# Kernel optimization log

Measured on AMD Instinct MI355X. Metric: run time of the kernel, lower is better.

The kernel has to match this reference:

```python
import jax, jax.numpy as jnp
import numpy as np

D = 1024   # cfg.hid (downscaled from 8192)
M = 20000  # cfg.mem_c // 2 (downscaled)
B, LQ = 4, 8
PLAST_S = 0.05
IMPORTANCE = 1.0


def mha_shared_kv(q, kv_k, kv_v, Wi, bi, Wo, bo, nheads):
    """torch nn.MultiheadAttention (batch_first) with batch-shared K/V.
    q: [B,Lq,D]; kv_k/kv_v: [Lk,D] shared across batch (avoids the .repeat()
    materialization in the original torch code while computing identical math)."""
    dh = D // nheads
    Wq, Wk, Wv = jnp.split(Wi, 3, axis=0)
    bq, bk, bv = jnp.split(bi, 3)
    qp = (jnp.einsum('bqd,ed->bqe', q, Wq) + bq) * (dh ** -0.5)
    kp = kv_k @ Wk.T + bk              # [Lk,D]
    vp = kv_v @ Wv.T + bv              # [Lk,D]
    qh = qp.reshape(q.shape[0], q.shape[1], nheads, dh)      # [B,Lq,h,dh]
    kh = kp.reshape(kp.shape[0], nheads, dh)                 # [Lk,h,dh]
    vh = vp.reshape(vp.shape[0], nheads, dh)                 # [Lk,h,dh]
    scores = jnp.einsum('bqhd,khd->bhqk', qh, kh)            # [B,h,Lq,Lk]
    attn = jax.nn.softmax(scores, axis=-1)
    ctx = jnp.einsum('bhqk,khd->bqhd', attn, vh)
    ctx = ctx.reshape(q.shape[0], q.shape[1], D)
    return ctx @ Wo.T + bo


def setup_inputs() -> dict:
    key = jax.random.key(0)
    ks = jax.random.split(key, 16)
    s = 0.02
    return {
        'q':    jax.random.normal(ks[0], (B, LQ, D), jnp.float32),
        'data': jax.random.normal(ks[1], (B, D), jnp.float32),
        'ek':   jax.random.normal(ks[2], (M, D), jnp.float32),
        'ev':   jax.random.normal(ks[3], (M, D), jnp.float32),
        'sk':   jax.random.normal(ks[4], (M, D), jnp.float32),
        'sv':   jax.random.normal(ks[5], (M, D), jnp.float32),
        'wm':   jax.random.normal(ks[6], (10, D), jnp.float32),
        'Wi_e': jax.random.normal(ks[7], (3 * D, D), jnp.float32) * s,
        'bi_e': jnp.zeros((3 * D,), jnp.float32),
        'Wo_e': jax.random.normal(ks[8], (D, D), jnp.float32) * s,
        'bo_e': jnp.zeros((D,), jnp.float32),
        'Wi_s': jax.random.normal(ks[9], (3 * D, D), jnp.float32) * s,
        'bi_s': jnp.zeros((3 * D,), jnp.float32),
        'Wo_s': jax.random.normal(ks[10], (D, D), jnp.float32) * s,
        'bo_s': jnp.zeros((D,), jnp.float32),
        'Wi_w': jax.random.normal(ks[11], (3 * D, D), jnp.float32) * s,
        'bi_w': jnp.zeros((3 * D,), jnp.float32),
        'Wo_w': jax.random.normal(ks[12], (D, D), jnp.float32) * s,
        'bo_w': jnp.zeros((D,), jnp.float32),
        'Wrp':  jax.random.normal(ks[13], (D, 3 * D), jnp.float32) * s,
        'brp':  jnp.zeros((D,), jnp.float32),
        'eu':   jnp.zeros((M,), jnp.float32),
    }


def reference(q, data, ek, ev, sk, sv, wm,
              Wi_e, bi_e, Wo_e, bo_e,
              Wi_s, bi_s, Wo_s, bo_s,
              Wi_w, bi_w, Wo_w, bo_w,
              Wrp, brp, eu):
    # ---- NeuroMemory.read ----
    e_r = mha_shared_kv(q, ek, ev, Wi_e, bi_e, Wo_e, bo_e, 16)
    s_r = mha_shared_kv(q, sk, sv, Wi_s, bi_s, Wo_s, bo_s, 16)
    w_r = mha_shared_kv(q, wm, wm, Wi_w, bi_w, Wo_w, bo_w, 8)
    read_out = jnp.concatenate([e_r, s_r, w_r], axis=-1) @ Wrp.T + brp  # [B,Lq,D]

    # ---- NeuroMemory.write (episodic, Hebbian plasticity update) ----
    scores = data @ ek.T                       # [B,M]
    probs = jax.nn.softmax(scores, axis=-1)    # [B,M]
    upd = probs * (PLAST_S * IMPORTANCE)       # [B,M]
    u = upd.mean(axis=0)[:, None]              # [M,1] (batch-mean update strength)
    d = data.mean(axis=0)[None, :]             # [1,D]
    new_ek = ek * (1.0 - u) + d * u            # [M,D]
    new_ev = ev * (1.0 - u) + d * u            # [M,D]
    new_eu = eu * 0.99 + jax.lax.stop_gradient(probs.sum(axis=0))  # [M]
    return (read_out, new_ek, new_ev, new_eu)
```

## Files before the change

kernel.cpp:

```cpp
#include <hip/hip_runtime.h>
#include <hip/hip_fp16.h>
#include <hip/hip_bf16.h>
#include <cstdint>
#include <cstddef>

#define D_HID 1024
#define MEM_M 20000
#define NBATCH 4
#define BL 32
#define NROWS 512
#define SROWS_E 516
#define SROWS_S 512
#define BK 32
#define LDT 40
#define PV_NC 16

typedef __attribute__((ext_vector_type(8))) short short8;
typedef __attribute__((ext_vector_type(4))) float f32x4;
typedef __attribute__((ext_vector_type(4))) unsigned short us4;

__device__ inline ushort f2bf(float f) {
    __hip_bfloat16 b = __float2bfloat16(f);
    return *reinterpret_cast<ushort*>(&b);
}
__device__ inline float h2f(ushort u) {
    __half h; *reinterpret_cast<ushort*>(&h) = u; return __half2float(h);
}

struct SkDesc  { const float* A; const float* B; int K; int M; };
struct SkDescs { SkDesc d[5]; };
struct RdDesc  { const float* bias; float* dst; int M; int ldc; float alpha; };
struct RdDescs { RdDesc d[5]; };

__device__ __forceinline__ void skinny_body(const SkDesc dd, float* __restrict__ part,
                                            int gk, int k0, int n0, int tid)
{
    __shared__ float As[32][132];
    __shared__ float Bs[64][129];
    const int K = dd.K, M = dd.M;
    {
        const int r = tid >> 3, cbl = (tid & 7) * 16;
        if (r < M) {
            const float* src = dd.A + (size_t)r * K + k0 + cbl;
            #pragma unroll
            for (int i = 0; i < 4; ++i) {
                const float4 v = *(const float4*)(src + i * 4);
                As[r][cbl + i * 4 + 0] = v.x; As[r][cbl + i * 4 + 1] = v.y;
                As[r][cbl + i * 4 + 2] = v.z; As[r][cbl + i * 4 + 3] = v.w;
            }
        } else {
            #pragma unroll
            for (int i = 0; i < 16; ++i) As[r][cbl + i] = 0.f;
        }
    }
    {
        const int r = tid >> 2, cbl = (tid & 3) * 32;
        const float* src = dd.B + (size_t)(n0 + r) * K + k0 + cbl;
        #pragma unroll
        for (int i = 0; i < 8; ++i) {
            const float4 v = *(const float4*)(src + i * 4);
            Bs[r][cbl + i * 4 + 0] = v.x; Bs[r][cbl + i * 4 + 1] = v.y;
            Bs[r][cbl + i * 4 + 2] = v.z; Bs[r][cbl + i * 4 + 3] = v.w;
        }
    }
    __syncthreads();
    const int n = tid & 63, mg = tid >> 6;
    float acc[8];
    #pragma unroll
    for (int i = 0; i < 8; ++i) acc[i] = 0.f;
    #pragma unroll 4
    for (int k = 0; k < 128; k += 4) {
        const float b0 = Bs[n][k + 0], b1 = Bs[n][k + 1];
        const float b2 = Bs[n][k + 2], b3 = Bs[n][k + 3];
        #pragma unroll
        for (int i = 0; i < 8; ++i) {
            const float4 a = *(const float4*)&As[mg * 8 + i][k];
            acc[i] = fmaf(a.x, b0, fmaf(a.y, b1, fmaf(a.z, b2, fmaf(a.w, b3, acc[i]))));
        }
    }
    #pragma unroll
    for (int i = 0; i < 8; ++i)
        part[((size_t)gk * 32 + mg * 8 + i) * 1024 + n0 + n] = acc[i];
}

__global__ __launch_bounds__(256)
void k_skinny(SkDescs ds, float* __restrict__ part)
{
    skinny_body(ds.d[blockIdx.z], part,
                blockIdx.z * gridDim.y + blockIdx.y,
                blockIdx.y * 128, blockIdx.x * 64, threadIdx.x);
}

__global__ __launch_bounds__(256)
void k_head(SkDescs ds, float* __restrict__ part,
            const float* __restrict__ ek, const float* __restrict__ sk,
            ushort* __restrict__ kvb)
{
    const int bx = blockIdx.x;
    const int tid = threadIdx.x;
    if (bx < 640) {
        const int g = bx >> 7;
        const int rem = bx & 127;
        const int kc = rem >> 4;
        const int n0 = (rem & 15) * 64;
        skinny_body(ds.d[g], part, g * 8 + kc, kc * 128, n0, tid);
    } else {
        const size_t nchunks = (size_t)2 * MEM_M * D_HID / 8;
        for (size_t i = (size_t)(bx - 640) * 256 + tid; i < nchunks;
             i += (size_t)1408 * 256) {
            const size_t base = i * 8;
            const float* src = (base < (size_t)MEM_M * D_HID)
                             ? (ek + base) : (sk + base - (size_t)MEM_M * D_HID);
            const float4 v0 = *(const float4*)(src);
            const float4 v1 = *(const float4*)(src + 4);
            alignas(16) ushort o[8];
            o[0] = f2bf(v0.x); o[1] = f2bf(v0.y); o[2] = f2bf(v0.z); o[3] = f2bf(v0.w);
            o[4] = f2bf(v1.x); o[5] = f2bf(v1.y); o[6] = f2bf(v1.z); o[7] = f2bf(v1.w);
            *(short8*)(kvb + base) = *(const short8*)o;
        }
    }
}

__global__ __launch_bounds__(256)
void k_skred(RdDescs ds, const float* __restrict__ part, int nkc)
{
    const int g = blockIdx.y;
    const int m = blockIdx.x;
    const RdDesc dd = ds.d[g];
    if (m >= dd.M) return;
    const int c = threadIdx.x * 4;
    float4 s = make_float4(0.f, 0.f, 0.f, 0.f);
    for (int kc = 0; kc < nkc; ++kc) {
        const float4 v = *(const float4*)&part[((size_t)(g * nkc + kc) * 32 + m) * 1024 + c];
        s.x += v.x; s.y += v.y; s.z += v.z; s.w += v.w;
    }
    const float4 b = *(const float4*)(dd.bias + c);
    float4 o;
    o.x = (s.x + b.x) * dd.alpha; o.y = (s.y + b.y) * dd.alpha;
    o.z = (s.z + b.z) * dd.alpha; o.w = (s.w + b.w) * dd.alpha;
    *(float4*)(dd.dst + (size_t)m * dd.ldc + c) = o;
}

__global__ __launch_bounds__(256)
void mfma_scores(const ushort* __restrict__ A_e, const ushort* __restrict__ ekb,
                 const ushort* __restrict__ A_s, const ushort* __restrict__ skb,
                 __half* __restrict__ S_e, __half* __restrict__ S_s,
                 const float* __restrict__ c0_e, const float* __restrict__ c0_s)
{
    __shared__ ushort As[2][128][LDT];
    __shared__ ushort Bs[2][128][LDT];
    const int tid = threadIdx.x;
    const int i = blockIdx.x + 9 * blockIdx.y;
    const int xcd = i & 7, idx = i >> 3;
    const int wg = (xcd < 5 ? xcd * 177 : 885 + (xcd - 5) * 176) + idx;
    const int mi = wg % 9, nbk = wg / 9;
    const int bank = (mi >= 5);
    const int m0 = (bank ? (mi - 5) : mi) * 128;
    const int n0 = nbk * 128;
    const ushort* __restrict__ A = bank ? A_s : A_e;
    const ushort* __restrict__ B = bank ? skb : ekb;
    __half* __restrict__ S = bank ? S_s : S_e;
    const float* __restrict__ c0 = bank ? c0_s : c0_e;
    const int Mreal = bank ? SROWS_S : SROWS_E;

    const int wid = tid >> 6, lane = tid & 63;
    const int wr = (wid >> 1) * 64, wc = (wid & 1) * 64;
    const int l15 = lane & 15, l4 = lane >> 4;

    const int srow = tid >> 1;
    const int ac = (tid & 1) * 16;
    int gbrow = n0 + srow; if (gbrow > MEM_M - 1) gbrow = MEM_M - 1;
    const ushort* Ap = A + (size_t)(m0 + srow) * 1024 + ac;
    const ushort* Bp = B + (size_t)gbrow * 1024 + ac;

    f32x4 acc[4][4];
    const f32x4 fz = {0.f, 0.f, 0.f, 0.f};
    #pragma unroll
    for (int ii = 0; ii < 4; ++ii)
        #pragma unroll
        for (int j = 0; j < 4; ++j) acc[ii][j] = fz;

    auto MF = [&](int bu) {
        short8 a[4], b[4];
        #pragma unroll
        for (int f = 0; f < 4; ++f) {
            a[f] = *(const short8*)&As[bu][wr + f * 16 + l15][l4 * 8];
            b[f] = *(const short8*)&Bs[bu][wc + f * 16 + l15][l4 * 8];
        }
        #pragma unroll
        for (int ii = 0; ii < 4; ++ii)
            #pragma unroll
            for (int j = 0; j < 4; ++j)
                acc[ii][j] = __builtin_amdgcn_mfma_f32_16x16x32_bf16(a[ii], b[j], acc[ii][j], 0, 0, 0);
    };

    short8 a00, a01, b00, b01;
    short8 a10, a11, b10, b11;

#define SC_LOAD0(KT) { a00 = *(const short8*)(Ap + (KT)); a01 = *(const short8*)(Ap + (KT) + 8); \
                       b00 = *(const short8*)(Bp + (KT)); b01 = *(const short8*)(Bp + (KT) + 8); }
#define SC_LOAD1(KT) { a10 = *(const short8*)(Ap + (KT)); a11 = *(const short8*)(Ap + (KT) + 8); \
                       b10 = *(const short8*)(Bp + (KT)); b11 = *(const short8*)(Bp + (KT) + 8); }
#define SC_STORE0(BU) { *(short8*)&As[BU][srow][ac] = a00; *(short8*)&As[BU][srow][ac + 8] = a01; \
                        *(short8*)&Bs[BU][srow][ac] = b00; *(short8*)&Bs[BU][srow][ac + 8] = b01; }
#define SC_STORE1(BU) { *(short8*)&As[BU][srow][ac] = a10; *(short8*)&As[BU][srow][ac + 8] = a11; \
                        *(short8*)&Bs[BU][srow][ac] = b10; *(short8*)&Bs[BU][srow][ac + 8] = b11; }

    SC_LOAD0(0);
    SC_LOAD1(32);
    SC_STORE0(0);
    __syncthreads();
    for (int it = 0; it < 16; ++it) {
        const int kt = it * 64;
        if (it < 15) SC_LOAD0(kt + 64);
        MF(0);
        SC_STORE1(1);
        __syncthreads();
        if (it < 15) SC_LOAD1(kt + 96);
        MF(1);
        if (it < 15) SC_STORE0(0);
        __syncthreads();
    }
#undef SC_LOAD0
#undef SC_LOAD1
#undef SC_STORE0
#undef SC_STORE1

    #pragma unroll
    for (int ii = 0; ii < 4; ++ii) {
        #pragma unroll
        for (int r = 0; r < 4; ++r) {
            const int row = m0 + wr + ii * 16 + l4 * 4 + r;
            if (row >= Mreal) continue;
            const float cr = c0[row];
            #pragma unroll
            for (int j = 0; j < 4; ++j) {
                const int col = n0 + wc + j * 16 + l15;
                if (col < MEM_M)
                    S[(size_t)row * MEM_M + col] = __float2half(acc[ii][j][r] + cr);
            }
        }
    }
}

__global__ __launch_bounds__(256)
void mfma_pv(const ushort* __restrict__ P_e, const ushort* __restrict__ P_s,
             const float* __restrict__ ev, const float* __restrict__ sv,
             float* __restrict__ part)
{
    __shared__ ushort As[2][128][LDT];
    __shared__ ushort Bs[2][128][LDT];
    const int tid = threadIdx.x;
    const int z = blockIdx.z;
    const int bank = z >> 4, c = z & 15;
    const ushort* __restrict__ P = bank ? P_s : P_e;
    const float* __restrict__ V = bank ? sv : ev;
    const int m0 = blockIdx.y * 128, n0 = blockIdx.x * 128;
    const int ks0 = (c * 625) / PV_NC, ks1 = ((c + 1) * 625) / PV_NC;
    const int wid = tid >> 6, lane = tid & 63;
    const int wr = (wid >> 1) * 64, wc = (wid & 1) * 64;
    const int l15 = lane & 15, l4 = lane >> 4;
    const int kb = (tid & 7) * 4, nb2 = (tid >> 3) * 4;
    const int srow = tid >> 1, ac = (tid & 1) * 16;
    const ushort* Pp = P + (size_t)(m0 + srow) * MEM_M + ac;
    const float*  Vp = V + (size_t)n0 + nb2;

    f32x4 acc[4][4];
    const f32x4 fz = {0.f, 0.f, 0.f, 0.f};
    #pragma unroll
    for (int i = 0; i < 4; ++i)
        #pragma unroll
        for (int j = 0; j < 4; ++j) acc[i][j] = fz;

    auto MF = [&](int bu) {
        short8 a[4], b[4];
        #pragma unroll
        for (int f = 0; f < 4; ++f) {
            a[f] = *(const short8*)&As[bu][wr + f * 16 + l15][l4 * 8];
            b[f] = *(const short8*)&Bs[bu][wc + f * 16 + l15][l4 * 8];
        }
        #pragma unroll
        for (int i = 0; i < 4; ++i)
            #pragma unroll
            for (int j = 0; j < 4; ++j)
                acc[i][j] = __builtin_amdgcn_mfma_f32_16x16x32_bf16(a[i], b[j], acc[i][j], 0, 0, 0);
    };

    short8 pa00, pa01, pa10, pa11;
    float4 q00, q01, q02, q03, q10, q11, q12, q13;

#define PV_LOAD0(T) { const int kt = (T) * 32; \
    pa00 = *(const short8*)(Pp + kt); pa01 = *(const short8*)(Pp + kt + 8); \
    q00 = *(const float4*)(Vp + (size_t)(kt + kb + 0) * 1024); \
    q01 = *(const float4*)(Vp + (size_t)(kt + kb + 1) * 1024); \
    q02 = *(const float4*)(Vp + (size_t)(kt + kb + 2) * 1024); \
    q03 = *(const float4*)(Vp + (size_t)(kt + kb + 3) * 1024); }
#define PV_LOAD1(T) { const int kt = (T) * 32; \
    pa10 = *(const short8*)(Pp + kt); pa11 = *(const short8*)(Pp + kt + 8); \
    q10 = *(const float4*)(Vp + (size_t)(kt + kb + 0) * 1024); \
    q11 = *(const float4*)(Vp + (size_t)(kt + kb + 1) * 1024); \
    q12 = *(const float4*)(Vp + (size_t)(kt + kb + 2) * 1024); \
    q13 = *(const float4*)(Vp + (size_t)(kt + kb + 3) * 1024); }
#define PV_STORE0(BU) { \
    *(short8*)&As[BU][srow][ac] = pa00; *(short8*)&As[BU][srow][ac + 8] = pa01; \
    us4 w; \
    w.x = f2bf(q00.x); w.y = f2bf(q01.x); w.z = f2bf(q02.x); w.w = f2bf(q03.x); \
    *(us4*)&Bs[BU][nb2 + 0][kb] = w; \
    w.x = f2bf(q00.y); w.y = f2bf(q01.y); w.z = f2bf(q02.y); w.w = f2bf(q03.y); \
    *(us4*)&Bs[BU][nb2 + 1][kb] = w; \
    w.x = f2bf(q00.z); w.y = f2bf(q01.z); w.z = f2bf(q02.z); w.w = f2bf(q03.z); \
    *(us4*)&Bs[BU][nb2 + 2][kb] = w; \
    w.x = f2bf(q00.w); w.y = f2bf(q01.w); w.z = f2bf(q02.w); w.w = f2bf(q03.w); \
    *(us4*)&Bs[BU][nb2 + 3][kb] = w; }
#define PV_STORE1(BU) { \
    *(short8*)&As[BU][srow][ac] = pa10; *(short8*)&As[BU][srow][ac + 8] = pa11; \
    us4 w; \
    w.x = f2bf(q10.x); w.y = f2bf(q11.x); w.z = f2bf(q12.x); w.w = f2bf(q13.x); \
    *(us4*)&Bs[BU][nb2 + 0][kb] = w; \
    w.x = f2bf(q10.y); w.y = f2bf(q11.y); w.z = f2bf(q12.y); w.w = f2bf(q13.y); \
    *(us4*)&Bs[BU][nb2 + 1][kb] = w; \
    w.x = f2bf(q10.z); w.y = f2bf(q11.z); w.z = f2bf(q12.z); w.w = f2bf(q13.z); \
    *(us4*)&Bs[BU][nb2 + 2][kb] = w; \
    w.x = f2bf(q10.w); w.y = f2bf(q11.w); w.z = f2bf(q12.w); w.w = f2bf(q13.w); \
    *(us4*)&Bs[BU][nb2 + 3][kb] = w; }

    PV_LOAD0(ks0);
    if (ks0 + 1 < ks1) PV_LOAD1(ks0 + 1);
    PV_STORE0(0);
    __syncthreads();
    for (int t = ks0; t < ks1; t += 2) {
        if (t + 2 < ks1) PV_LOAD0(t + 2);
        MF(0);
        if (t + 1 < ks1) PV_STORE1(1);
        __syncthreads();
        if (t + 1 < ks1) {
            if (t + 3 < ks1) PV_LOAD1(t + 3);
            MF(1);
            if (t + 2 < ks1) PV_STORE0(0);
            __syncthreads();
        }
    }
#undef PV_LOAD0
#undef PV_LOAD1
#undef PV_STORE0
#undef PV_STORE1

    float* __restrict__ po = part + (size_t)z * NROWS * 1024;
    #pragma unroll
    for (int i = 0; i < 4; ++i)
        #pragma unroll
        for (int r = 0; r < 4; ++r) {
            const int row = m0 + wr + i * 16 + l4 * 4 + r;
            #pragma unroll
            for (int j = 0; j < 4; ++j) {
                const int col = n0 + wc + j * 16 + l15;
                po[(size_t)row * 1024 + col] = acc[i][j][r];
            }
        }
}

__global__ __launch_bounds__(256)
void k_T(const float* __restrict__ qp,
         const float* __restrict__ Wi_e, const float* __restrict__ bi_e,
         const float* __restrict__ Wi_s, const float* __restrict__ bi_s,
         ushort* __restrict__ A_e, float* __restrict__ c0_e,
         ushort* __restrict__ A_s, float* __restrict__ c0_s,
         const float* __restrict__ data, float* __restrict__ dmean)
{
    const int bq = blockIdx.x;
    const int tid = threadIdx.x;
    if (bq >= 128) {
        if (bq < 252) {
            const int row = SROWS_E + (bq - 128);
            us4 z4; z4.x = 0; z4.y = 0; z4.z = 0; z4.w = 0;
            *(us4*)(A_e + (size_t)row * 1024 + tid * 4) = z4;
        } else {
            for (int t = tid; t < D_HID; t += 256) {
                float s = 0.f;
                #pragma unroll
                for (int b = 0; b < NBATCH; ++b) s += data[b * D_HID + t];
                dmean[t] = 0.25f * s;
                #pragma unroll
                for (int b = 0; b < NBATCH; ++b)
                    A_e[(size_t)(NROWS + b) * 1024 + t] = f2bf(data[b * D_HID + t]);
            }
            if (tid < NBATCH) c0_e[NROWS + tid] = 0.f;
        }
        return;
    }
    const int bank = bq >> 6;
    const int h = (bq >> 2) & 15;
    const int q4 = bq & 3;
    const float* qpB = qp + (size_t)bank * BL * D_HID;
    const float* Wk = (bank ? Wi_s : Wi_e) + (size_t)D_HID * D_HID;
    const float* bk = (bank ? bi_s : bi_e) + D_HID;
    ushort* T  = bank ? A_s : A_e;
    float* c0 = bank ? c0_s : c0_e;

    __shared__ float qs[32][64];
    for (int i = tid; i < 32 * 64; i += 256) {
        const int r = i >> 6, j = i & 63;
        qs[r][j] = qpB[(size_t)r * D_HID + h * 64 + j];
    }
    __syncthreads();
    const int e = q4 * 256 + tid;
    float acc[32];
    #pragma unroll
    for (int r = 0; r < 32; ++r) acc[r] = 0.f;
    for (int j = 0; j < 64; ++j) {
        const float w = Wk[(size_t)(h * 64 + j) * D_HID + e];
        #pragma unroll
        for (int r = 0; r < 32; ++r) acc[r] = fmaf(qs[r][j], w, acc[r]);
    }
    #pragma unroll
    for (int r = 0; r < 32; ++r) T[(size_t)(r * 16 + h) * 1024 + e] = f2bf(acc[r]);
    if (q4 == 0 && tid < 32) {
        float s = 0.f;
        for (int j = 0; j < 64; ++j) s += qs[tid][j] * bk[h * 64 + j];
        c0[tid * 16 + h] = s;
    }
}

__global__ __launch_bounds__(256)
void k_softmax(__half* __restrict__ S_e, __half* __restrict__ S_s,
               float* __restrict__ mrow, float* __restrict__ lrow)
{
    const int row = blockIdx.x;
    ushort* p = (row < SROWS_E) ? (ushort*)(S_e + (size_t)row * MEM_M)
                                : (ushort*)(S_s + (size_t)(row - SROWS_E) * MEM_M);
    const bool conv = (row < SROWS_E) ? (row < NROWS) : true;
    __shared__ float red_m[256];
    __shared__ float red_l[256];
    const int tid = threadIdx.x;
    float m = -3.0e38f, l = 0.f;
    for (int c = tid; c < MEM_M / 8; c += 256) {
        alignas(16) ushort t[8];
        *(short8*)t = *(const short8*)(p + c * 8);
        float v[8];
        #pragma unroll
        for (int j = 0; j < 8; ++j) v[j] = h2f(t[j]);
        float cm = v[0];
        #pragma unroll
        for (int j = 1; j < 8; ++j) cm = fmaxf(cm, v[j]);
        const float nm = fmaxf(m, cm);
        float s = 0.f;
        #pragma unroll
        for (int j = 0; j < 8; ++j) s += __expf(v[j] - nm);
        l = l * __expf(m - nm) + s;
        m = nm;
    }
    red_m[tid] = m; red_l[tid] = l; __syncthreads();
    for (int s = 128; s > 0; s >>= 1) {
        if (tid < s) {
            const float m2 = fmaxf(red_m[tid], red_m[tid + s]);
            red_l[tid] = red_l[tid] * __expf(red_m[tid] - m2)
                       + red_l[tid + s] * __expf(red_m[tid + s] - m2);
            red_m[tid] = m2;
        }
        __syncthreads();
    }
    const float rm = red_m[0];
    if (conv) {
        for (int c = tid; c < MEM_M / 8; c += 256) {
            alignas(16) ushort t[8];
            *(short8*)t = *(const short8*)(p + c * 8);
            alignas(16) ushort o[8];
            #pragma unroll
            for (int j = 0; j < 8; ++j) o[j] = f2bf(__expf(h2f(t[j]) - rm));
            *(short8*)(p + c * 8) = *(const short8*)o;
        }
    }
    if (tid == 0) { mrow[row] = rm; lrow[row] = red_l[0]; }
}

__global__ __launch_bounds__(256)
void k_uk(const __half* __restrict__ S_e,
          const float* __restrict__ mrow, const float* __restrict__ lrow,
          const float* __restrict__ eu,
          float* __restrict__ u, float* __restrict__ out_eu)
{
    const int k = blockIdx.x * 256 + threadIdx.x;
    if (k >= MEM_M) return;
    float sp = 0.f;
    #pragma unroll
    for (int b = 0; b < NBATCH; ++b) {
        const int row = NROWS + b;
        sp += __expf(__half2float(S_e[(size_t)row * MEM_M + k]) - mrow[row]) / lrow[row];
    }
    u[k] = 0.05f * 0.25f * sp;
    out_eu[k] = eu[k] * 0.99f + sp;
}

__global__ __launch_bounds__(256)
void k_pvred_upd(const float* __restrict__ part, const float* __restrict__ lrow,
                 float* __restrict__ R,
                 const float* __restrict__ ev, const float* __restrict__ u,
                 const float* __restrict__ dmean, float* __restrict__ out_ev)
{
    const int tid = threadIdx.x;
    if (blockIdx.x < 1024) {
        const size_t perb4 = (size_t)NROWS * 1024 / 4;
        const size_t i = (size_t)blockIdx.x * 256 + tid;
        const int bank = i >= perb4;
        const size_t off4 = i - (size_t)bank * perb4;
        const int m = (int)(off4 >> 8);
        const float inv = 1.f / lrow[bank ? (SROWS_E + m) : m];
        const float4* p = (const float4*)part + (size_t)bank * PV_NC * perb4 + off4;
        float4 s = make_float4(0.f, 0.f, 0.f, 0.f);
        #pragma unroll
        for (int c = 0; c < PV_NC; ++c) {
            const float4 v = p[(size_t)c * perb4];
            s.x += v.x; s.y += v.y; s.z += v.z; s.w += v.w;
        }
        s.x *= inv; s.y *= inv; s.z *= inv; s.w *= inv;
        ((float4*)R)[i] = s;
    } else {
        const int bid = blockIdx.x - 1024;
        const size_t n4 = (size_t)MEM_M * D_HID / 4;
        for (size_t i = (size_t)bid * 256 + tid; i < n4; i += (size_t)1024 * 256) {
            const int k = (int)(i >> 8);
            const int c = (int)(i & 255);
            const float uk = u[k];
            const float om = 1.f - uk;
            const float4 dd = ((const float4*)dmean)[c];
            const float4 b = ((const float4*)ev)[i];
            float4 ob;
            ob.x = b.x * om + dd.x * uk; ob.y = b.y * om + dd.y * uk;
            ob.z = b.z * om + dd.z * uk; ob.w = b.w * om + dd.w * uk;
            ((float4*)out_ev)[i] = ob;
        }
    }
}

__global__ __launch_bounds__(256)
void k_tail(const float* __restrict__ R,
            const float* __restrict__ Wi_e, const float* __restrict__ bi_e,
            const float* __restrict__ Wi_s, const float* __restrict__ bi_s,
            float* __restrict__ ctx,
            const float* __restrict__ qp, const float* __restrict__ kpw,
            const float* __restrict__ vpw,
            const float* __restrict__ ek, const float* __restrict__ u,
            const float* __restrict__ dmean, float* __restrict__ out_ek)
{
    __shared__ float sm[12384];
    const int tid = threadIdx.x;
    const int bx = blockIdx.x;
    if (bx < 32) {
        const int bank = bx >> 4;
        const int h = bx & 15;
        const float* Rb = R + (size_t)bank * NROWS * D_HID;
        const float* Wv = (bank ? Wi_s : Wi_e) + (size_t)2 * D_HID * D_HID;
        const float* bv = (bank ? bi_s : bi_e) + 2 * D_HID;
        float* cb = ctx + (size_t)bank * BL * D_HID;
        float (*Rs)[129] = (float(*)[129])sm;
        float (*Ws)[129] = (float(*)[129])(sm + 32 * 129);
        const int j = tid & 63;
        const int g = tid >> 6;
        float acc[8];
        #pragma unroll
        for (int i = 0; i < 8; ++i) acc[i] = 0.f;
        for (int ec = 0; ec < D_HID; ec += 128) {
            for (int i = tid; i < 32 * 128; i += 256) {
                const int r = i >> 7, e = i & 127;
                Rs[r][e] = Rb[(size_t)(r * 16 + h) * D_HID + ec + e];
            }
            for (int i = tid; i < 64 * 128; i += 256) {
                const int r = i >> 7, e = i & 127;
                Ws[r][e] = Wv[(size_t)(h * 64 + r) * D_HID + ec + e];
            }
            __syncthreads();
            for (int e = 0; e < 128; ++e) {
                const float w = Ws[j][e];
                #pragma unroll
                for (int i = 0; i < 8; ++i)
                    acc[i] = fmaf(Rs[g + 4 * i][e], w, acc[i]);
            }
            __syncthreads();
        }
        #pragma unroll
        for (int i = 0; i < 8; ++i) {
            const int bl = g + 4 * i;
            cb[(size_t)bl * D_HID + h * 64 + j] = acc[i] + bv[h * 64 + j];
        }
    } else if (bx < 64) {
        const int bl = bx - 32;
        float* q = sm;
        float (*kp)[1024] = (float(*)[1024])(sm + 1024);
        float (*pp)[10] = (float(*)[10])(sm + 1024 + 10240);
        const float* qrow = qp + (size_t)(2 * BL + bl) * D_HID;
        for (int i = tid; i < D_HID; i += 256) q[i] = qrow[i];
        for (int i = tid; i < 10 * D_HID; i += 256) kp[i >> 10][i & 1023] = kpw[i];
        __syncthreads();
        if (tid < 80) {
            const int h = tid / 10, k = tid % 10;
            float s = 0.f;
            for (int jj = 0; jj < 128; ++jj) s += q[h * 128 + jj] * kp[k][h * 128 + jj];
            pp[h][k] = s;
        }
        __syncthreads();
        if (tid < 8) {
            float m = -3.0e38f;
            for (int k = 0; k < 10; ++k) m = fmaxf(m, pp[tid][k]);
            float e[10]; float l = 0.f;
            for (int k = 0; k < 10; ++k) { e[k] = __expf(pp[tid][k] - m); l += e[k]; }
            const float inv = 1.f / l;
            for (int k = 0; k < 10; ++k) pp[tid][k] = e[k] * inv;
        }
        __syncthreads();
        float* cw = ctx + (size_t)(2 * BL + bl) * D_HID;
        for (int f = tid; f < D_HID; f += 256) {
            const int h = f >> 7;
            float s = 0.f;
            #pragma unroll
            for (int k = 0; k < 10; ++k) s += pp[h][k] * vpw[(size_t)k * D_HID + f];
            cw[f] = s;
        }
    } else {
        const int bid = bx - 64;
        const size_t n4 = (size_t)MEM_M * D_HID / 4;
        for (size_t i = (size_t)bid * 256 + tid; i < n4; i += (size_t)1024 * 256) {
            const int k = (int)(i >> 8);
            const int c = (int)(i & 255);
            const float uk = u[k];
            const float om = 1.f - uk;
            const float4 dd = ((const float4*)dmean)[c];
            const float4 a = ((const float4*)ek)[i];
            float4 oa;
            oa.x = a.x * om + dd.x * uk; oa.y = a.y * om + dd.y * uk;
            oa.z = a.z * om + dd.z * uk; oa.w = a.w * om + dd.w * uk;
            ((float4*)out_ek)[i] = oa;
        }
    }
}

extern "C" void kernel_launch(void* const* d_in, const int* in_sizes, int n_in,
                              void* d_out, int out_size, void* d_ws, size_t ws_size,
                              hipStream_t stream)
{
    (void)in_sizes; (void)n_in; (void)out_size; (void)ws_size;
    const float* q    = (const float*)d_in[0];
    const float* data = (const float*)d_in[1];
    const float* ek   = (const float*)d_in[2];
    const float* ev   = (const float*)d_in[3];
    const float* sk   = (const float*)d_in[4];
    const float* sv   = (const float*)d_in[5];
    const float* wm   = (const float*)d_in[6];
    const float* Wi_e = (const float*)d_in[7];
    const float* bi_e = (const float*)d_in[8];
    const float* Wo_e = (const float*)d_in[9];
    const float* bo_e = (const float*)d_in[10];
    const float* Wi_s = (const float*)d_in[11];
    const float* bi_s = (const float*)d_in[12];
    const float* Wo_s = (const float*)d_in[13];
    const float* bo_s = (const float*)d_in[14];
    const float* Wi_w = (const float*)d_in[15];
    const float* bi_w = (const float*)d_in[16];
    const float* Wo_w = (const float*)d_in[17];
    const float* bo_w = (const float*)d_in[18];
    const float* Wrp  = (const float*)d_in[19];
    const float* brp  = (const float*)d_in[20];
    const float* eu   = (const float*)d_in[21];

    float* out = (float*)d_out;
    float* out_read = out;
    float* out_ek = out + 32768;
    float* out_ev = out_ek + 20480000;
    float* out_eu = out_ev + 20480000;

    float* ws    = (float*)d_ws;
    float* qp    = ws;
    float* A_e   = qp + 98304;
    float* A_s   = A_e + 655360;
    float* c0_e  = A_s + 524288;
    float* c0_s  = c0_e + 640;
    float* dmean = c0_s + 512;
    float* u     = dmean + 1024;
    float* mrow  = u + 20480;
    float* lrow  = mrow + 1032;
    float* kpw   = lrow + 1032;
    float* vpw   = kpw + 10240;
    float* ctx   = vpw + 10240;
    float* cat   = ctx + 98304;
    float* skpart = cat + 98304;
    float* Rbuf  = skpart;

    ushort* A_e16 = (ushort*)A_e;
    ushort* A_s16 = (ushort*)A_s;

    ushort* ekb = (ushort*)out_ek;
    ushort* skb = ekb + (size_t)MEM_M * D_HID;
    float* part = out_ek;
    __half* S_e = (__half*)out_ev;
    __half* S_s = S_e + (size_t)SROWS_E * MEM_M;

    const dim3 b256(256);
    const float sc16 = 0.125f;
    const float sc8  = 0.08838834764831845f;

    SkDescs s1;
    s1.d[0] = {q,  Wi_e,            1024, 32};
    s1.d[1] = {q,  Wi_s,            1024, 32};
    s1.d[2] = {q,  Wi_w,            1024, 32};
    s1.d[3] = {wm, Wi_w + 1048576,  1024, 10};
    s1.d[4] = {wm, Wi_w + 2097152,  1024, 10};
    k_head<<<2048, b256, 0, stream>>>(s1, skpart, ek, sk, ekb);
    RdDescs r1;
    r1.d[0] = {bi_e,        qp,         32, 1024, sc16};
    r1.d[1] = {bi_s,        qp + 32768, 32, 1024, sc16};
    r1.d[2] = {bi_w,        qp + 65536, 32, 1024, sc8};
    r1.d[3] = {bi_w + 1024, kpw,        10, 1024, 1.f};
    r1.d[4] = {bi_w + 2048, vpw,        10, 1024, 1.f};
    k_skred<<<dim3(32, 5), b256, 0, stream>>>(r1, skpart, 8);

    k_T<<<253, b256, 0, stream>>>(qp, Wi_e, bi_e, Wi_s, bi_s,
                                  A_e16, c0_e, A_s16, c0_s, data, dmean);

    mfma_scores<<<dim3(9, 157), b256, 0, stream>>>(A_e16, ekb, A_s16, skb,
                                                   S_e, S_s, c0_e, c0_s);

    k_softmax<<<SROWS_E + SROWS_S, b256, 0, stream>>>(S_e, S_s, mrow, lrow);
    k_uk<<<79, b256, 0, stream>>>(S_e, mrow, lrow, eu, u, out_eu);

    mfma_pv<<<dim3(8, 4, 2 * PV_NC), b256, 0, stream>>>((const ushort*)S_e, (const ushort*)S_s,
                                                        ev, sv, part);

    k_pvred_upd<<<2048, b256, 0, stream>>>(part, lrow, Rbuf, ev, u, dmean, out_ev);

    k_tail<<<1088, b256, 0, stream>>>(Rbuf, Wi_e, bi_e, Wi_s, bi_s, ctx,
                                      qp, kpw, vpw, ek, u, dmean, out_ek);

    SkDescs s2;
    s2.d[0] = {ctx,         Wo_e, 1024, 32};
    s2.d[1] = {ctx + 32768, Wo_s, 1024, 32};
    s2.d[2] = {ctx + 65536, Wo_w, 1024, 32};
    s2.d[3] = {ctx,         Wo_e, 1024, 32};
    s2.d[4] = {ctx,         Wo_e, 1024, 32};
    k_skinny<<<dim3(16, 8, 3), b256, 0, stream>>>(s2, skpart);
    RdDescs r2;
    r2.d[0] = {bo_e, cat,        32, 3072, 1.f};
    r2.d[1] = {bo_s, cat + 1024, 32, 3072, 1.f};
    r2.d[2] = {bo_w, cat + 2048, 32, 3072, 1.f};
    r2.d[3] = r2.d[0];
    r2.d[4] = r2.d[0];
    k_skred<<<dim3(32, 3), b256, 0, stream>>>(r2, skpart, 8);

    SkDescs s3;
    s3.d[0] = {cat, Wrp, 3072, 32};
    s3.d[1] = s3.d[0]; s3.d[2] = s3.d[0]; s3.d[3] = s3.d[0]; s3.d[4] = s3.d[0];
    k_skinny<<<dim3(16, 24, 1), b256, 0, stream>>>(s3, skpart);
    RdDescs r3;
    r3.d[0] = {brp, out_read, 32, 1024, 1.f};
    r3.d[1] = r3.d[0]; r3.d[2] = r3.d[0]; r3.d[3] = r3.d[0]; r3.d[4] = r3.d[0];
    k_skred<<<dim3(32, 1), b256, 0, stream>>>(r3, skpart, 24);
}
```

Before: 498.4 us.

## Load MFMA operands directly from global memory, bypassing LDS, and remap PV workgroups to XCDs

In the scores GEMM, each lane now loads its MFMA A and B fragments straight from global memory into registers with register double-buffering. This removes the LDS staging and both __syncthreads per step. In the PV GEMM, the P operand is loaded directly per lane in the same way, and only V still goes through LDS for its bf16 transpose. The PV grid is also remapped so that consecutive workgroups sharing inputs land on the same XCD. The cost is that each wave reloads overlapping tiles through the cache instead of sharing them via LDS, using more L2 bandwidth and registers.

```diff
diff --git a/kernel.cpp b/kernel.cpp
--- a/kernel.cpp
+++ b/kernel.cpp
@@ -147,8 +147,6 @@
                  __half* __restrict__ S_e, __half* __restrict__ S_s,
                  const float* __restrict__ c0_e, const float* __restrict__ c0_s)
 {
-    __shared__ ushort As[2][128][LDT];
-    __shared__ ushort Bs[2][128][LDT];
     const int tid = threadIdx.x;
     const int i = blockIdx.x + 9 * blockIdx.y;
     const int xcd = i & 7, idx = i >> 3;
@@ -167,11 +165,14 @@
     const int wr = (wid >> 1) * 64, wc = (wid & 1) * 64;
     const int l15 = lane & 15, l4 = lane >> 4;
 
-    const int srow = tid >> 1;
-    const int ac = (tid & 1) * 16;
-    int gbrow = n0 + srow; if (gbrow > MEM_M - 1) gbrow = MEM_M - 1;
-    const ushort* Ap = A + (size_t)(m0 + srow) * 1024 + ac;
-    const ushort* Bp = B + (size_t)gbrow * 1024 + ac;
+    const ushort* Ap[4];
+    const ushort* Bp[4];
+    #pragma unroll
+    for (int f = 0; f < 4; ++f) {
+        Ap[f] = A + (size_t)(m0 + wr + f * 16 + l15) * 1024 + l4 * 8;
+        int r = n0 + wc + f * 16 + l15; if (r > MEM_M - 1) r = MEM_M - 1;
+        Bp[f] = B + (size_t)r * 1024 + l4 * 8;
+    }
 
     f32x4 acc[4][4];
     const f32x4 fz = {0.f, 0.f, 0.f, 0.f};
@@ -180,51 +181,38 @@
         #pragma unroll
         for (int j = 0; j < 4; ++j) acc[ii][j] = fz;
 
-    auto MF = [&](int bu) {
-        short8 a[4], b[4];
+    short8 a0[4], b0[4], a1[4], b1[4];
+    #pragma unroll
+    for (int f = 0; f < 4; ++f) {
+        a0[f] = *(const short8*)Ap[f];
+        b0[f] = *(const short8*)Bp[f];
+    }
+    for (int it = 0; it < 16; ++it) {
+        const int k1 = it * 64 + 32;
         #pragma unroll
         for (int f = 0; f < 4; ++f) {
-            a[f] = *(const short8*)&As[bu][wr + f * 16 + l15][l4 * 8];
-            b[f] = *(const short8*)&Bs[bu][wc + f * 16 + l15][l4 * 8];
+            a1[f] = *(const short8*)(Ap[f] + k1);
+            b1[f] = *(const short8*)(Bp[f] + k1);
         }
         #pragma unroll
         for (int ii = 0; ii < 4; ++ii)
             #pragma unroll
             for (int j = 0; j < 4; ++j)
-                acc[ii][j] = __builtin_amdgcn_mfma_f32_16x16x32_bf16(a[ii], b[j], acc[ii][j], 0, 0, 0);
-    };
-
-    short8 a00, a01, b00, b01;
-    short8 a10, a11, b10, b11;
-
-#define SC_LOAD0(KT) { a00 = *(const short8*)(Ap + (KT)); a01 = *(const short8*)(Ap + (KT) + 8); \
-                       b00 = *(const short8*)(Bp + (KT)); b01 = *(const short8*)(Bp + (KT) + 8); }
-#define SC_LOAD1(KT) { a10 = *(const short8*)(Ap + (KT)); a11 = *(const short8*)(Ap + (KT) + 8); \
-                       b10 = *(const short8*)(Bp + (KT)); b11 = *(const short8*)(Bp + (KT) + 8); }
-#define SC_STORE0(BU) { *(short8*)&As[BU][srow][ac] = a00; *(short8*)&As[BU][srow][ac + 8] = a01; \
-                        *(short8*)&Bs[BU][srow][ac] = b00; *(short8*)&Bs[BU][srow][ac + 8] = b01; }
-#define SC_STORE1(BU) { *(short8*)&As[BU][srow][ac] = a10; *(short8*)&As[BU][srow][ac + 8] = a11; \
-                        *(short8*)&Bs[BU][srow][ac] = b10; *(short8*)&Bs[BU][srow][ac + 8] = b11; }
-
-    SC_LOAD0(0);
-    SC_LOAD1(32);
-    SC_STORE0(0);
-    __syncthreads();
-    for (int it = 0; it < 16; ++it) {
-        const int kt = it * 64;
-        if (it < 15) SC_LOAD0(kt + 64);
-        MF(0);
-        SC_STORE1(1);
-        __syncthreads();
-        if (it < 15) SC_LOAD1(kt + 96);
-        MF(1);
-        if (it < 15) SC_STORE0(0);
-        __syncthreads();
-    }
-#undef SC_LOAD0
-#undef SC_LOAD1
-#undef SC_STORE0
-#undef SC_STORE1
+                acc[ii][j] = __builtin_amdgcn_mfma_f32_16x16x32_bf16(a0[ii], b0[j], acc[ii][j], 0, 0, 0);
+        if (it < 15) {
+            const int k2 = k1 + 32;
+            #pragma unroll
+            for (int f = 0; f < 4; ++f) {
+                a0[f] = *(const short8*)(Ap[f] + k2);
+                b0[f] = *(const short8*)(Bp[f] + k2);
+            }
+        }
+        #pragma unroll
+        for (int ii = 0; ii < 4; ++ii)
+            #pragma unroll
+            for (int j = 0; j < 4; ++j)
+                acc[ii][j] = __builtin_amdgcn_mfma_f32_16x16x32_bf16(a1[ii], b1[j], acc[ii][j], 0, 0, 0);
+    }
 
     #pragma unroll
     for (int ii = 0; ii < 4; ++ii) {
@@ -248,113 +236,99 @@
              const float* __restrict__ ev, const float* __restrict__ sv,
              float* __restrict__ part)
 {
-    __shared__ ushort As[2][128][LDT];
     __shared__ ushort Bs[2][128][LDT];
     const int tid = threadIdx.x;
-    const int z = blockIdx.z;
+    const int bid = blockIdx.x + 8 * (blockIdx.y + 4 * blockIdx.z);
+    const int wgs = (bid & 7) * 128 + (bid >> 3);
+    const int nI = wgs & 7, mI = (wgs >> 3) & 3;
+    const int z = wgs >> 5;
     const int bank = z >> 4, c = z & 15;
     const ushort* __restrict__ P = bank ? P_s : P_e;
     const float* __restrict__ V = bank ? sv : ev;
-    const int m0 = blockIdx.y * 128, n0 = blockIdx.x * 128;
+    const int m0 = mI * 128, n0 = nI * 128;
     const int ks0 = (c * 625) / PV_NC, ks1 = ((c + 1) * 625) / PV_NC;
     const int wid = tid >> 6, lane = tid & 63;
     const int wr = (wid >> 1) * 64, wc = (wid & 1) * 64;
     const int l15 = lane & 15, l4 = lane >> 4;
     const int kb = (tid & 7) * 4, nb2 = (tid >> 3) * 4;
-    const int srow = tid >> 1, ac = (tid & 1) * 16;
-    const ushort* Pp = P + (size_t)(m0 + srow) * MEM_M + ac;
-    const float*  Vp = V + (size_t)n0 + nb2;
+    const float* Vp = V + (size_t)n0 + nb2;
+    const ushort* Pp[4];
+    #pragma unroll
+    for (int f = 0; f < 4; ++f)
+        Pp[f] = P + (size_t)(m0 + wr + f * 16 + l15) * MEM_M + l4 * 8;
 
     f32x4 acc[4][4];
     const f32x4 fz = {0.f, 0.f, 0.f, 0.f};
     #pragma unroll
-    for (int i = 0; i < 4; ++i)
-        #pragma unroll
-        for (int j = 0; j < 4; ++j) acc[i][j] = fz;
-
-    auto MF = [&](int bu) {
-        short8 a[4], b[4];
-        #pragma unroll
-        for (int f = 0; f < 4; ++f) {
-            a[f] = *(const short8*)&As[bu][wr + f * 16 + l15][l4 * 8];
-            b[f] = *(const short8*)&Bs[bu][wc + f * 16 + l15][l4 * 8];
-        }
-        #pragma unroll
-        for (int i = 0; i < 4; ++i)
+    for (int ii = 0; ii < 4; ++ii)
+        #pragma unroll
+        for (int j = 0; j < 4; ++j) acc[ii][j] = fz;
+
+    short8 aF[4], aN[4];
+    float4 q0[4], q1[4];
+
+    auto PLOADF = [&](short8* d, int T) {
+        #pragma unroll
+        for (int f = 0; f < 4; ++f) d[f] = *(const short8*)(Pp[f] + T * 32);
+    };
+    auto VLOAD = [&](float4* qq, int T) {
+        #pragma unroll
+        for (int r = 0; r < 4; ++r)
+            qq[r] = *(const float4*)(Vp + (size_t)(T * 32 + kb + r) * 1024);
+    };
+    auto VSTORE = [&](int BU, const float4* qq) {
+        us4 w;
+        w.x = f2bf(qq[0].x); w.y = f2bf(qq[1].x); w.z = f2bf(qq[2].x); w.w = f2bf(qq[3].x);
+        *(us4*)&Bs[BU][nb2 + 0][kb] = w;
+        w.x = f2bf(qq[0].y); w.y = f2bf(qq[1].y); w.z = f2bf(qq[2].y); w.w = f2bf(qq[3].y);
+        *(us4*)&Bs[BU][nb2 + 1][kb] = w;
+        w.x = f2bf(qq[0].z); w.y = f2bf(qq[1].z); w.z = f2bf(qq[2].z); w.w = f2bf(qq[3].z);
+        *(us4*)&Bs[BU][nb2 + 2][kb] = w;
+        w.x = f2bf(qq[0].w); w.y = f2bf(qq[1].w); w.z = f2bf(qq[2].w); w.w = f2bf(qq[3].w);
+        *(us4*)&Bs[BU][nb2 + 3][kb] = w;
+    };
+    auto MSTEP = [&](const short8* af, int BU) {
+        short8 b[4];
+        #pragma unroll
+        for (int f = 0; f < 4; ++f)
+            b[f] = *(const short8*)&Bs[BU][wc + f * 16 + l15][l4 * 8];
+        #pragma unroll
+        for (int ii = 0; ii < 4; ++ii)
             #pragma unroll
             for (int j = 0; j < 4; ++j)
-                acc[i][j] = __builtin_amdgcn_mfma_f32_16x16x32_bf16(a[i], b[j], acc[i][j], 0, 0, 0);
+                acc[ii][j] = __builtin_amdgcn_mfma_f32_16x16x32_bf16(af[ii], b[j], acc[ii][j], 0, 0, 0);
     };
 
-    short8 pa00, pa01, pa10, pa11;
-    float4 q00, q01, q02, q03, q10, q11, q12, q13;
-
-#define PV_LOAD0(T) { const int kt = (T) * 32; \
-    pa00 = *(const short8*)(Pp + kt); pa01 = *(const short8*)(Pp + kt + 8); \
-    q00 = *(const float4*)(Vp + (size_t)(kt + kb + 0) * 1024); \
-    q01 = *(const float4*)(Vp + (size_t)(kt + kb + 1) * 1024); \
-    q02 = *(const float4*)(Vp + (size_t)(kt + kb + 2) * 1024); \
-    q03 = *(const float4*)(Vp + (size_t)(kt + kb + 3) * 1024); }
-#define PV_LOAD1(T) { const int kt = (T) * 32; \
-    pa10 = *(const short8*)(Pp + kt); pa11 = *(const short8*)(Pp + kt + 8); \
-    q10 = *(const float4*)(Vp + (size_t)(kt + kb + 0) * 1024); \
-    q11 = *(const float4*)(Vp + (size_t)(kt + kb + 1) * 1024); \
-    q12 = *(const float4*)(Vp + (size_t)(kt + kb + 2) * 1024); \
-    q13 = *(const float4*)(Vp + (size_t)(kt + kb + 3) * 1024); }
-#define PV_STORE0(BU) { \
-    *(short8*)&As[BU][srow][ac] = pa00; *(short8*)&As[BU][srow][ac + 8] = pa01; \
-    us4 w; \
-    w.x = f2bf(q00.x); w.y = f2bf(q01.x); w.z = f2bf(q02.x); w.w = f2bf(q03.x); \
-    *(us4*)&Bs[BU][nb2 + 0][kb] = w; \
-    w.x = f2bf(q00.y); w.y = f2bf(q01.y); w.z = f2bf(q02.y); w.w = f2bf(q03.y); \
-    *(us4*)&Bs[BU][nb2 + 1][kb] = w; \
-    w.x = f2bf(q00.z); w.y = f2bf(q01.z); w.z = f2bf(q02.z); w.w = f2bf(q03.z); \
-    *(us4*)&Bs[BU][nb2 + 2][kb] = w; \
-    w.x = f2bf(q00.w); w.y = f2bf(q01.w); w.z = f2bf(q02.w); w.w = f2bf(q03.w); \
-    *(us4*)&Bs[BU][nb2 + 3][kb] = w; }
-#define PV_STORE1(BU) { \
-    *(short8*)&As[BU][srow][ac] = pa10; *(short8*)&As[BU][srow][ac + 8] = pa11; \
-    us4 w; \
-    w.x = f2bf(q10.x); w.y = f2bf(q11.x); w.z = f2bf(q12.x); w.w = f2bf(q13.x); \
-    *(us4*)&Bs[BU][nb2 + 0][kb] = w; \
-    w.x = f2bf(q10.y); w.y = f2bf(q11.y); w.z = f2bf(q12.y); w.w = f2bf(q13.y); \
-    *(us4*)&Bs[BU][nb2 + 1][kb] = w; \
-    w.x = f2bf(q10.z); w.y = f2bf(q11.z); w.z = f2bf(q12.z); w.w = f2bf(q13.z); \
-    *(us4*)&Bs[BU][nb2 + 2][kb] = w; \
-    w.x = f2bf(q10.w); w.y = f2bf(q11.w); w.z = f2bf(q12.w); w.w = f2bf(q13.w); \
-    *(us4*)&Bs[BU][nb2 + 3][kb] = w; }
-
-    PV_LOAD0(ks0);
-    if (ks0 + 1 < ks1) PV_LOAD1(ks0 + 1);
-    PV_STORE0(0);
+    PLOADF(aF, ks0);
+    VLOAD(q0, ks0);
+    VSTORE(0, q0);
+    if (ks0 + 1 < ks1) VLOAD(q1, ks0 + 1);
     __syncthreads();
     for (int t = ks0; t < ks1; t += 2) {
-        if (t + 2 < ks1) PV_LOAD0(t + 2);
-        MF(0);
-        if (t + 1 < ks1) PV_STORE1(1);
+        if (t + 2 < ks1) VLOAD(q0, t + 2);
+        if (t + 1 < ks1) PLOADF(aN, t + 1);
+        MSTEP(aF, 0);
+        if (t + 1 < ks1) VSTORE(1, q1);
         __syncthreads();
         if (t + 1 < ks1) {
-            if (t + 3 < ks1) PV_LOAD1(t + 3);
-            MF(1);
-            if (t + 2 < ks1) PV_STORE0(0);
+            if (t + 3 < ks1) VLOAD(q1, t + 3);
+            if (t + 2 < ks1) PLOADF(aF, t + 2);
+            MSTEP(aN, 1);
+            if (t + 2 < ks1) VSTORE(0, q0);
             __syncthreads();
         }
     }
-#undef PV_LOAD0
-#undef PV_LOAD1
-#undef PV_STORE0
-#undef PV_STORE1
 
     float* __restrict__ po = part + (size_t)z * NROWS * 1024;
     #pragma unroll
-    for (int i = 0; i < 4; ++i)
+    for (int ii = 0; ii < 4; ++ii)
         #pragma unroll
         for (int r = 0; r < 4; ++r) {
-            const int row = m0 + wr + i * 16 + l4 * 4 + r;
+            const int row = m0 + wr + ii * 16 + l4 * 4 + r;
             #pragma unroll
             for (int j = 0; j < 4; ++j) {
                 const int col = n0 + wc + j * 16 + l15;
-                po[(size_t)row * 1024 + col] = acc[i][j][r];
+                po[(size_t)row * 1024 + col] = acc[ii][j][r];
             }
         }
 }
```

Result: slower. 616.8 us (+23.8%).
